# Kernel optimization log

Hardware: AMD Instinct MI355X
Metric: run time of the kernel (lower is better)

## Reference

```python
import jax, jax.numpy as jnp
import numpy as np

# Mamba defaults (mamba_ssm): expand=2, d_state=16, d_conv=4, dt_rank=ceil(d_model/16)
D_MODEL = 256
DEPTH = 2
D_INNER = 2 * D_MODEL          # 512
D_STATE = 16
D_CONV = 4
DT_RANK = (D_MODEL + 15) // 16  # 16
BATCH = 2
SEQLEN = 2048


def setup_inputs() -> dict:
    key = jax.random.key(0)
    ks = jax.random.split(key, 12)
    s = 0.02
    x = jax.random.normal(ks[0], (BATCH, SEQLEN, D_MODEL), jnp.float32)
    ln_w = jnp.ones((DEPTH, D_MODEL), jnp.float32)
    ln_b = jnp.zeros((DEPTH, D_MODEL), jnp.float32)
    in_proj_w = jax.random.normal(ks[1], (DEPTH, 2 * D_INNER, D_MODEL), jnp.float32) * s
    conv_w = jax.random.normal(ks[2], (DEPTH, D_INNER, 1, D_CONV), jnp.float32) * 0.2
    conv_b = jnp.zeros((DEPTH, D_INNER), jnp.float32)
    x_proj_w = jax.random.normal(ks[3], (DEPTH, DT_RANK + 2 * D_STATE, D_INNER), jnp.float32) * s
    dt_proj_w = jax.random.normal(ks[4], (DEPTH, D_INNER, DT_RANK), jnp.float32) * (DT_RANK ** -0.5)
    # dt bias initialized so softplus(bias) ~ U(1e-3, 1e-1), as in mamba_ssm
    dt = jnp.exp(jax.random.uniform(ks[5], (DEPTH, D_INNER)) * (np.log(0.1) - np.log(1e-3)) + np.log(1e-3))
    dt_proj_b = dt + jnp.log(-jnp.expm1(-dt))  # inverse softplus
    A_log = jnp.log(jnp.broadcast_to(jnp.arange(1, D_STATE + 1, dtype=jnp.float32), (DEPTH, D_INNER, D_STATE)))
    D_param = jnp.ones((DEPTH, D_INNER), jnp.float32)
    out_proj_w = jax.random.normal(ks[6], (DEPTH, D_MODEL, D_INNER), jnp.float32) * s
    return {"x": x, "ln_w": ln_w, "ln_b": ln_b, "in_proj_w": in_proj_w,
            "conv_w": conv_w, "conv_b": conv_b, "x_proj_w": x_proj_w,
            "dt_proj_w": dt_proj_w, "dt_proj_b": dt_proj_b, "A_log": A_log,
            "D_param": D_param, "out_proj_w": out_proj_w}


def _layernorm(x, w, b, eps=1e-5):
    mu = jnp.mean(x, axis=-1, keepdims=True)
    var = jnp.var(x, axis=-1, keepdims=True)
    return (x - mu) * jax.lax.rsqrt(var + eps) * w + b


def _mamba_block(x, lw, lb, ipw, cw, cb, xpw, dpw, dpb, alog, dpar, opw):
    # x: [B, L, D]; returns x + Mamba(LN(x))  (residual handled by caller of stack)
    B, L, _ = x.shape
    h = _layernorm(x, lw, lb)
    xz = jnp.einsum('bld,ed->ble', h, ipw)            # [B, L, 2*d_inner]
    xi, z = jnp.split(xz, 2, axis=-1)
    # depthwise causal conv1d
    xc = jnp.transpose(xi, (0, 2, 1))                 # [B, d_inner, L]
    xc = jax.lax.conv_general_dilated(
        xc, cw, window_strides=(1,), padding=[(D_CONV - 1, 0)],
        feature_group_count=D_INNER, dimension_numbers=('NCH', 'OIH', 'NCH'))
    xc = jax.nn.silu(xc + cb[None, :, None])
    xc = jnp.transpose(xc, (0, 2, 1))                 # [B, L, d_inner]
    # input-dependent SSM parameters
    dbl = jnp.einsum('bld,ed->ble', xc, xpw)          # [B, L, dt_rank+2*d_state]
    dt = dbl[..., :DT_RANK]
    Bs = dbl[..., DT_RANK:DT_RANK + D_STATE]          # [B, L, d_state]
    Cs = dbl[..., DT_RANK + D_STATE:]                 # [B, L, d_state]
    delta = jax.nn.softplus(jnp.einsum('blr,dr->bld', dt, dpw) + dpb)  # [B, L, d_inner]
    A = -jnp.exp(alog)                                # [d_inner, d_state]
    dA = jnp.exp(jnp.einsum('bld,dn->bldn', delta, A))
    dBu = jnp.einsum('bld,bln,bld->bldn', delta, Bs, xc)
    # sequential selective scan over time (time-major)
    dA_t = jnp.moveaxis(dA, 1, 0)
    dBu_t = jnp.moveaxis(dBu, 1, 0)
    C_t = jnp.moveaxis(Cs, 1, 0)
    h0 = jnp.zeros((B, D_INNER, D_STATE), x.dtype)
    def step(hprev, inp):
        dA_, dBu_, C_ = inp
        hnew = dA_ * hprev + dBu_                     # [B, d_inner, d_state]
        y = jnp.einsum('bdn,bn->bd', hnew, C_)        # [B, d_inner]
        return hnew, y
    _, ys = jax.lax.scan(step, h0, (dA_t, dBu_t, C_t))
    y = jnp.moveaxis(ys, 0, 1)                        # [B, L, d_inner]
    y = y + xc * dpar
    y = y * jax.nn.silu(z)
    out = jnp.einsum('ble,de->bld', y, opw)           # [B, L, D]
    return x + out


def reference(x, ln_w, ln_b, in_proj_w, conv_w, conv_b, x_proj_w,
              dt_proj_w, dt_proj_b, A_log, D_param, out_proj_w):
    for i in range(DEPTH):
        x = _mamba_block(x, ln_w[i], ln_b[i], in_proj_w[i], conv_w[i], conv_b[i],
                         x_proj_w[i], dt_proj_w[i], dt_proj_b[i], A_log[i],
                         D_param[i], out_proj_w[i])
    return x
```

## Files before the change

### kernel.cpp

```cpp
#include <hip/hip_runtime.h>
#include <hip/hip_bf16.h>
#include <math.h>

#define D_MODEL 256
#define DEPTH 2
#define D_INNER 512
#define D_STATE 16
#define D_CONV 4
#define DT_RANK 16
#define BATCH 2
#define SEQLEN 2048
#define MROWS (BATCH * SEQLEN)

#define LCH 8
#define NCH 512
#define CPB 256

typedef __attribute__((ext_vector_type(8))) short bf16x8;
typedef __attribute__((ext_vector_type(4))) float f32x4;

__device__ __forceinline__ float silu(float v) {
    return v / (1.0f + __expf(-v));
}

__device__ __forceinline__ ushort f2bf(float f) {
    union { float f; unsigned u; } v; v.f = f;
    unsigned r = v.u + 0x7FFFu + ((v.u >> 16) & 1u);
    return (ushort)(r >> 16);
}

__device__ __forceinline__ float bf2f(ushort u) {
    union { unsigned u; float f; } v; v.u = ((unsigned)u) << 16;
    return v.f;
}

__device__ __forceinline__ float softplus_f(float x) {
    return (x > 20.f) ? x : __logf(1.f + __expf(x));
}

#define XS_STR 260
#define HS_STR 264
#define XC_STR 520

__global__ __launch_bounds__(256) void k_cvt(
    const float* __restrict__ ipw, const float* __restrict__ xpw,
    const float* __restrict__ opw, ushort* __restrict__ ipwT,
    ushort* __restrict__ xpwT, ushort* __restrict__ opwT)
{
    size_t tid = (size_t)blockIdx.x * 256 + threadIdx.x;
    {
        int lyr = (int)(tid >> 16), rem = (int)(tid & 65535);
        int n = rem >> 6, k = (rem & 63) * 4;
        float4 v = *(const float4*)(ipw + ((size_t)lyr * 1024 + n) * 256 + k);
        int nt = n >> 4, r = n & 15, kt = k >> 5, c = k & 31;
        ushort4 o = { f2bf(v.x), f2bf(v.y), f2bf(v.z), f2bf(v.w) };
        *(ushort4*)(ipwT + (size_t)lyr * 262144 + (nt * 8 + kt) * 512 + r * 32 + c) = o;
    }
    if (tid < 12288) {
        int lyr = (int)(tid / 6144), rem = (int)(tid % 6144);
        int n = rem >> 7, k = (rem & 127) * 4;
        float4 v = *(const float4*)(xpw + ((size_t)lyr * 48 + n) * 512 + k);
        int nt = n >> 4, r = n & 15, kt = k >> 5, c = k & 31;
        ushort4 o = { f2bf(v.x), f2bf(v.y), f2bf(v.z), f2bf(v.w) };
        *(ushort4*)(xpwT + (size_t)lyr * 24576 + (nt * 16 + kt) * 512 + r * 32 + c) = o;
    }
    if (tid < 65536) {
        int lyr = (int)(tid >> 15), rem = (int)(tid & 32767);
        int n = rem >> 7, k = (rem & 127) * 4;
        float4 v = *(const float4*)(opw + ((size_t)lyr * 256 + n) * 512 + k);
        int nt = n >> 4, r = n & 15, kt = k >> 5, c = k & 31;
        ushort4 o = { f2bf(v.x), f2bf(v.y), f2bf(v.z), f2bf(v.w) };
        *(ushort4*)(opwT + (size_t)lyr * 131072 + (nt * 16 + kt) * 512 + r * 32 + c) = o;
    }
}

__global__ __launch_bounds__(512, 4) void k_front(
    const float* __restrict__ xin, const float* __restrict__ lnwL,
    const float* __restrict__ lnbL, const ushort* __restrict__ ipwT,
    const float* __restrict__ cwL, const float* __restrict__ cbL,
    const ushort* __restrict__ xpwT, const float* __restrict__ dpwL,
    const float* __restrict__ dpbL, const float* __restrict__ alogL,
    ushort* __restrict__ zsB, ushort* __restrict__ xcB,
    float* __restrict__ dbl, float* __restrict__ Ssum,
    float* __restrict__ sdsum)
{
    const int t = threadIdx.x, bid = blockIdx.x;
    const int lane = t & 63, w = t >> 6, l15 = lane & 15, quad = lane >> 4;
    __shared__ float  xs[11 * XS_STR];
    __shared__ ushort hs[16 * HS_STR];
    __shared__ ushort xi_s[11 * 512];
    __shared__ ushort xc_s[16 * XC_STR];
    __shared__ float  dbl_s[8 * 52];
    int m0 = bid * LCH;

    for (int i = t; i < 11 * 64; i += 512) {
        int r = i >> 6, c = (i & 63) * 4;
        int grow = m0 - 3 + r; if (grow < 0) grow = 0;
        float4 v = *(const float4*)(xin + (size_t)grow * D_MODEL + c);
        *(float4*)&xs[r * XS_STR + c] = v;
    }
    __syncthreads();

    if (t < 11 * 32) {
        int r = t >> 5, ci = t & 31;
        float s = 0.f, sq = 0.f;
        #pragma unroll
        for (int k = 0; k < 8; k++) {
            float v = xs[r * XS_STR + ci + 32 * k];
            s += v; sq += v * v;
        }
        #pragma unroll
        for (int off = 1; off < 32; off <<= 1) {
            s  += __shfl_xor(s, off, 32);
            sq += __shfl_xor(sq, off, 32);
        }
        float mu  = s * (1.0f / 256.f);
        float var = sq * (1.0f / 256.f) - mu * mu;
        float rst = rsqrtf(var + 1e-5f);
        #pragma unroll
        for (int k = 0; k < 8; k++) {
            int c = ci + 32 * k;
            float v = (xs[r * XS_STR + c] - mu) * rst * lnwL[c] + lnbL[c];
            hs[r * HS_STR + c] = f2bf(v);
        }
    }
    __syncthreads();

    {
        bf16x8 af[8];
        #pragma unroll
        for (int k8 = 0; k8 < 8; k8++)
            af[k8] = *(const bf16x8*)&hs[l15 * HS_STR + quad * 8 + k8 * 32];
        const ushort* wb = ipwT + (size_t)w * 64 * 512 + l15 * 32 + quad * 8;

        #pragma unroll
        for (int half = 0; half < 2; half++) {
            const ushort* wh = wb + (size_t)half * 4 * 8 * 512;
            f32x4 acc[4];
            #pragma unroll
            for (int f = 0; f < 4; f++) acc[f] = (f32x4){0.f, 0.f, 0.f, 0.f};
            bf16x8 bA[4], bB[4];
            #pragma unroll
            for (int f = 0; f < 4; f++) bA[f] = *(const bf16x8*)(wh + (f * 8) * 512);
            #pragma unroll
            for (int k8 = 0; k8 < 8; k8++) {
                bf16x8* cur = (k8 & 1) ? bB : bA;
                bf16x8* nxt = (k8 & 1) ? bA : bB;
                if (k8 < 7) {
                    #pragma unroll
                    for (int f = 0; f < 4; f++)
                        nxt[f] = *(const bf16x8*)(wh + (f * 8 + k8 + 1) * 512);
                }
                #pragma unroll
                for (int f = 0; f < 4; f++)
                    acc[f] = __builtin_amdgcn_mfma_f32_16x16x32_bf16(af[k8], cur[f], acc[f], 0, 0, 0);
            }
            #pragma unroll
            for (int f = 0; f < 4; f++) {
                int n = w * 128 + (half * 4 + f) * 16 + l15;
                if (n < 512) {
                    #pragma unroll
                    for (int r2 = 0; r2 < 4; r2++) {
                        int rl = quad * 4 + r2;
                        if (rl < 11) xi_s[rl * 512 + n] = f2bf(acc[f][r2]);
                    }
                } else {
                    #pragma unroll
                    for (int r2 = 0; r2 < 4; r2++) {
                        int rl = quad * 4 + r2;
                        if (rl >= 3 && rl < 11)
                            zsB[(size_t)(m0 + rl - 3) * D_INNER + (n - 512)] =
                                f2bf(silu(acc[f][r2]));
                    }
                }
            }
        }
    }
    __syncthreads();

    {
        float4 cw4 = *(const float4*)(cwL + t * 4);
        float cbv = cbL[t];
        #pragma unroll
        for (int rl = 0; rl < LCH; rl++) {
            int l = (m0 + rl) & (SEQLEN - 1);
            float s = cbv;
            if (l >= 3) s = fmaf(cw4.x, bf2f(xi_s[(rl + 0) * 512 + t]), s);
            if (l >= 2) s = fmaf(cw4.y, bf2f(xi_s[(rl + 1) * 512 + t]), s);
            if (l >= 1) s = fmaf(cw4.z, bf2f(xi_s[(rl + 2) * 512 + t]), s);
            s = fmaf(cw4.w, bf2f(xi_s[(rl + 3) * 512 + t]), s);
            ushort xcv = f2bf(silu(s));
            xc_s[rl * XC_STR + t] = xcv;
            xcB[(size_t)(m0 + rl) * D_INNER + t] = xcv;
        }
    }
    __syncthreads();

    if (w < 3) {
        const ushort* wb = xpwT + (size_t)w * 16 * 512 + l15 * 32 + quad * 8;
        bf16x8 bw[16];
        #pragma unroll
        for (int k8 = 0; k8 < 16; k8++)
            bw[k8] = *(const bf16x8*)(wb + k8 * 512);
        f32x4 acc = (f32x4){0.f, 0.f, 0.f, 0.f};
        #pragma unroll
        for (int k8 = 0; k8 < 16; k8++) {
            bf16x8 af = *(const bf16x8*)&xc_s[l15 * XC_STR + quad * 8 + k8 * 32];
            acc = __builtin_amdgcn_mfma_f32_16x16x32_bf16(af, bw[k8], acc, 0, 0, 0);
        }
        int n = w * 16 + l15;
        #pragma unroll
        for (int r2 = 0; r2 < 4; r2++) {
            int rl = quad * 4 + r2;
            if (rl < LCH) {
                dbl_s[rl * 52 + n] = acc[r2];
                dbl[(size_t)(m0 + rl) * 48 + n] = acc[r2];
            }
        }
    }
    __syncthreads();

    {
        float a[16], wdp[16];
        #pragma unroll
        for (int n = 0; n < 16; n++) a[n] = -__expf(alogL[(size_t)t * 16 + n]);
        *(float4*)&wdp[0]  = *(const float4*)(dpwL + (size_t)t * 16 + 0);
        *(float4*)&wdp[4]  = *(const float4*)(dpwL + (size_t)t * 16 + 4);
        *(float4*)&wdp[8]  = *(const float4*)(dpwL + (size_t)t * 16 + 8);
        *(float4*)&wdp[12] = *(const float4*)(dpwL + (size_t)t * 16 + 12);
        float bias = dpbL[t];
        float h[16];
        #pragma unroll
        for (int n = 0; n < 16; n++) h[n] = 0.f;
        float sd = 0.f;
        for (int j = 0; j < LCH; j++) {
            const float* dp = &dbl_s[j * 52];
            float d0 = 0.f, d1 = 0.f;
            #pragma unroll
            for (int r2 = 0; r2 < 8; r2++) {
                d0 = fmaf(dp[r2], wdp[r2], d0);
                d1 = fmaf(dp[8 + r2], wdp[8 + r2], d1);
            }
            float dl = softplus_f(bias + d0 + d1);
            float xv = bf2f(xc_s[j * XC_STR + t]);
            float u = dl * xv;
            sd += dl;
            #pragma unroll
            for (int n = 0; n < 16; n++)
                h[n] = fmaf(__expf(dl * a[n]), h[n], dp[16 + n] * u);
        }
        size_t sbase = (size_t)bid * 16 * D_INNER + t;
        #pragma unroll
        for (int n = 0; n < 16; n++) Ssum[sbase + (size_t)n * D_INNER] = h[n];
        sdsum[(size_t)bid * D_INNER + t] = sd;
    }
}

__global__ __launch_bounds__(512, 4) void k_comb(
    const float* __restrict__ alogL, const float* __restrict__ sdsum,
    float* __restrict__ Ssum)
{
    const int t = threadIdx.x, bid = blockIdx.x;
    __shared__ float S_l[32][17], sd_l[32][17];
    int ch32 = t & 31, seg = t >> 5;
    int chain = bid * 32 + ch32;
    int d = chain & 511;
    int n = (chain >> 9) & 15;
    int b = chain >> 13;
    float a = -__expf(alogL[(size_t)d * 16 + n]);
    int c0 = b * CPB + seg * 16;

    float s_r[16], sd_r[16];
    float S = 0.f, sdt = 0.f;
    #pragma unroll
    for (int j = 0; j < 16; j++) {
        size_t c = (size_t)(c0 + j);
        float s  = Ssum[(c * 16 + n) * D_INNER + d];
        float sd = sdsum[c * D_INNER + d];
        s_r[j] = s; sd_r[j] = sd;
        S = fmaf(__expf(a * sd), S, s);
        sdt += sd;
    }
    S_l[ch32][seg] = S;
    sd_l[ch32][seg] = sdt;
    __syncthreads();

    if (t < 32) {
        float hi = 0.f;
        #pragma unroll
        for (int g = 0; g < 16; g++) {
            float Sv = S_l[t][g], sdv = sd_l[t][g];
            S_l[t][g] = hi;
            hi = fmaf(__expf(a * sdv), hi, Sv);
        }
    }
    __syncthreads();

    float hi = S_l[ch32][seg];
    #pragma unroll
    for (int j = 0; j < 16; j++) {
        size_t c = (size_t)(c0 + j);
        if (!(j & 1))
            Ssum[(c * 16 + n) * D_INNER + d] = hi;
        hi = fmaf(__expf(a * sd_r[j]), hi, s_r[j]);
    }
}

__global__ __launch_bounds__(512, 2) void k_back(
    const float* __restrict__ dbl, const ushort* __restrict__ xcB,
    const ushort* __restrict__ zsB, const float* __restrict__ Ssum,
    const float* __restrict__ dpwL, const float* __restrict__ dpbL,
    const float* __restrict__ alogL, const float* __restrict__ dparL,
    const ushort* __restrict__ opwT, const float* __restrict__ xin,
    float* __restrict__ xout)
{
    const int t = threadIdx.x, bid = blockIdx.x;
    const int lane = t & 63, w = t >> 6, l15 = lane & 15, quad = lane >> 4;
    __shared__ ushort yy_s[16 * XC_STR];
    __shared__ float  dbl_l[16 * 48];
    int m0 = bid * 16;

    for (int i = t; i < 16 * 48; i += 512) dbl_l[i] = dbl[(size_t)m0 * 48 + i];

    ushort xcv[16], zsv[16];
    #pragma unroll
    for (int j = 0; j < 16; j++) {
        size_t rb = (size_t)(m0 + j) * D_INNER + t;
        xcv[j] = xcB[rb];
        zsv[j] = zsB[rb];
    }
    float h[16];
    {
        size_t sbase = ((size_t)(2 * bid) * 16) * D_INNER + t;
        #pragma unroll
        for (int n = 0; n < 16; n++) h[n] = Ssum[sbase + (size_t)n * D_INNER];
    }
    float a[16], wdp[16];
    #pragma unroll
    for (int n = 0; n < 16; n++) a[n] = -__expf(alogL[(size_t)t * 16 + n]);
    *(float4*)&wdp[0]  = *(const float4*)(dpwL + (size_t)t * 16 + 0);
    *(float4*)&wdp[4]  = *(const float4*)(dpwL + (size_t)t * 16 + 4);
    *(float4*)&wdp[8]  = *(const float4*)(dpwL + (size_t)t * 16 + 8);
    *(float4*)&wdp[12] = *(const float4*)(dpwL + (size_t)t * 16 + 12);
    float bias = dpbL[t];
    float Dd = dparL[t];
    __syncthreads();

    for (int j = 0; j < 16; j++) {
        const float* dp = &dbl_l[j * 48];
        float d0 = 0.f, d1 = 0.f;
        #pragma unroll
        for (int r2 = 0; r2 < 8; r2++) {
            d0 = fmaf(dp[r2], wdp[r2], d0);
            d1 = fmaf(dp[8 + r2], wdp[8 + r2], d1);
        }
        float dl = softplus_f(bias + d0 + d1);
        float xv = bf2f(xcv[j]);
        float gate = bf2f(zsv[j]);
        float u = dl * xv;
        float y0 = 0.f, y1 = 0.f, y2 = 0.f, y3 = 0.f;
        #pragma unroll
        for (int q = 0; q < 4; q++) {
            h[4 * q + 0] = fmaf(__expf(dl * a[4 * q + 0]), h[4 * q + 0], dp[16 + 4 * q + 0] * u);
            h[4 * q + 1] = fmaf(__expf(dl * a[4 * q + 1]), h[4 * q + 1], dp[16 + 4 * q + 1] * u);
            h[4 * q + 2] = fmaf(__expf(dl * a[4 * q + 2]), h[4 * q + 2], dp[16 + 4 * q + 2] * u);
            h[4 * q + 3] = fmaf(__expf(dl * a[4 * q + 3]), h[4 * q + 3], dp[16 + 4 * q + 3] * u);
            y0 = fmaf(h[4 * q + 0], dp[32 + 4 * q + 0], y0);
            y1 = fmaf(h[4 * q + 1], dp[32 + 4 * q + 1], y1);
            y2 = fmaf(h[4 * q + 2], dp[32 + 4 * q + 2], y2);
            y3 = fmaf(h[4 * q + 3], dp[32 + 4 * q + 3], y3);
        }
        float y = (y0 + y1) + (y2 + y3) + xv * Dd;
        yy_s[j * XC_STR + t] = f2bf(y * gate);
    }
    __syncthreads();

    {
        const ushort* wb = opwT + (size_t)w * 2 * 16 * 512 + l15 * 32 + quad * 8;
        f32x4 acc0 = (f32x4){0.f, 0.f, 0.f, 0.f};
        f32x4 acc1 = (f32x4){0.f, 0.f, 0.f, 0.f};
        bf16x8 bA0 = *(const bf16x8*)(wb + 0 * 512);
        bf16x8 bA1 = *(const bf16x8*)(wb + 16 * 512);
        bf16x8 bB0, bB1;
        #pragma unroll
        for (int k8 = 0; k8 < 16; k8++) {
            if (k8 < 15) {
                if (k8 & 1) { bA0 = *(const bf16x8*)(wb + (k8 + 1) * 512);
                              bA1 = *(const bf16x8*)(wb + (16 + k8 + 1) * 512); }
                else        { bB0 = *(const bf16x8*)(wb + (k8 + 1) * 512);
                              bB1 = *(const bf16x8*)(wb + (16 + k8 + 1) * 512); }
            }
            bf16x8 af = *(const bf16x8*)&yy_s[l15 * XC_STR + quad * 8 + k8 * 32];
            bf16x8 c0 = (k8 & 1) ? bB0 : bA0;
            bf16x8 c1 = (k8 & 1) ? bB1 : bA1;
            acc0 = __builtin_amdgcn_mfma_f32_16x16x32_bf16(af, c0, acc0, 0, 0, 0);
            acc1 = __builtin_amdgcn_mfma_f32_16x16x32_bf16(af, c1, acc1, 0, 0, 0);
        }
        #pragma unroll
        for (int f = 0; f < 2; f++) {
            int n = w * 32 + f * 16 + l15;
            const f32x4& acc = (f == 0) ? acc0 : acc1;
            #pragma unroll
            for (int r2 = 0; r2 < 4; r2++) {
                int row = m0 + quad * 4 + r2;
                xout[(size_t)row * D_MODEL + n] =
                    acc[r2] + xin[(size_t)row * D_MODEL + n];
            }
        }
    }
}

extern "C" void kernel_launch(void* const* d_in, const int* in_sizes, int n_in,
                              void* d_out, int out_size, void* d_ws, size_t ws_size,
                              hipStream_t stream)
{
    const float* x    = (const float*)d_in[0];
    const float* lnw  = (const float*)d_in[1];
    const float* lnb  = (const float*)d_in[2];
    const float* ipw  = (const float*)d_in[3];
    const float* cw   = (const float*)d_in[4];
    const float* cb   = (const float*)d_in[5];
    const float* xpw  = (const float*)d_in[6];
    const float* dpw  = (const float*)d_in[7];
    const float* dpb  = (const float*)d_in[8];
    const float* alog = (const float*)d_in[9];
    const float* dpar = (const float*)d_in[10];
    const float* opw  = (const float*)d_in[11];
    float* out = (float*)d_out;

    char* p = (char*)d_ws;
    auto alloc = [&](size_t bytes) { char* r = p; p += (bytes + 255) & ~(size_t)255; return r; };
    ushort* zsB   = (ushort*)alloc((size_t)MROWS * D_INNER * 2);
    ushort* xcB   = (ushort*)alloc((size_t)MROWS * D_INNER * 2);
    float*  dbl   = (float*)alloc((size_t)MROWS * 48 * 4);
    float*  Ssum  = (float*)alloc((size_t)NCH * 16 * D_INNER * 4);
    float*  sdsum = (float*)alloc((size_t)NCH * D_INNER * 4);
    ushort* ipwT  = (ushort*)alloc((size_t)DEPTH * 262144 * 2);
    ushort* xpwT  = (ushort*)alloc((size_t)DEPTH * 24576 * 2);
    ushort* opwT  = (ushort*)alloc((size_t)DEPTH * 131072 * 2);

    k_cvt<<<512, 256, 0, stream>>>(ipw, xpw, opw, ipwT, xpwT, opwT);

    for (int lyr = 0; lyr < DEPTH; lyr++) {
        const float* xin = (lyr == 0) ? x : out;
        float* xout = out;
        const float* alogL = alog + (size_t)lyr * D_INNER * D_STATE;
        const float* dpwL  = dpw + (size_t)lyr * D_INNER * DT_RANK;
        const float* dpbL  = dpb + lyr * D_INNER;

        k_front<<<NCH, 512, 0, stream>>>(
            xin, lnw + lyr * D_MODEL, lnb + lyr * D_MODEL,
            ipwT + (size_t)lyr * 262144,
            cw + (size_t)lyr * D_INNER * D_CONV, cb + lyr * D_INNER,
            xpwT + (size_t)lyr * 24576, dpwL, dpbL, alogL,
            zsB, xcB, dbl, Ssum, sdsum);

        k_comb<<<512, 512, 0, stream>>>(alogL, sdsum, Ssum);

        k_back<<<NCH / 2, 512, 0, stream>>>(
            dbl, xcB, zsB, Ssum, dpwL, dpbL, alogL,
            dpar + lyr * D_INNER,
            opwT + (size_t)lyr * 131072, xin, xout);
    }
}
```

Measured before the change: 204.0 us.

## Fuse depthwise causal conv into in_proj MFMA epilogue via lane shuffles

```diff
diff --git a/kernel.cpp b/kernel.cpp
--- a/kernel.cpp
+++ b/kernel.cpp
@@ -88,11 +88,14 @@
     const int lane = t & 63, w = t >> 6, l15 = lane & 15, quad = lane >> 4;
     __shared__ float  xs[11 * XS_STR];
     __shared__ ushort hs[16 * HS_STR];
-    __shared__ ushort xi_s[11 * 512];
     __shared__ ushort xc_s[16 * XC_STR];
     __shared__ float  dbl_s[8 * 52];
+    __shared__ float4 cw_s[512];
+    __shared__ float  cb_s[512];
     int m0 = bid * LCH;
 
+    cw_s[t] = *(const float4*)(cwL + t * 4);
+    cb_s[t] = cbL[t];
     for (int i = t; i < 11 * 64; i += 512) {
         int r = i >> 6, c = (i & 63) * 4;
         int grow = m0 - 3 + r; if (grow < 0) grow = 0;
@@ -155,16 +158,42 @@
                 for (int f = 0; f < 4; f++)
                     acc[f] = __builtin_amdgcn_mfma_f32_16x16x32_bf16(af[k8], cur[f], acc[f], 0, 0, 0);
             }
-            #pragma unroll
-            for (int f = 0; f < 4; f++) {
-                int n = w * 128 + (half * 4 + f) * 16 + l15;
-                if (n < 512) {
-                    #pragma unroll
-                    for (int r2 = 0; r2 < 4; r2++) {
-                        int rl = quad * 4 + r2;
-                        if (rl < 11) xi_s[rl * 512 + n] = f2bf(acc[f][r2]);
+
+            if (w < 4) {
+                #pragma unroll
+                for (int f = 0; f < 4; f++) {
+                    int n = w * 128 + (half * 4 + f) * 16 + l15;
+                    float x0 = acc[f][0], x1 = acc[f][1], x2 = acc[f][2], x3 = acc[f][3];
+                    float p1 = __shfl_up(x1, 16);
+                    float p2 = __shfl_up(x2, 16);
+                    float p3 = __shfl_up(x3, 16);
+                    float4 cwv = cw_s[n];
+                    float cbv = cb_s[n];
+                    int jb = quad * 4 - 3;
+                    #define EMIT(JOFF, T0, T1, T2, T3)                          \
+                    {   int j = jb + (JOFF);                                    \
+                        if (j >= 0 && j < 8) {                                  \
+                            int l = (m0 + j) & (SEQLEN - 1);                    \
+                            float s = cbv;                                      \
+                            if (l >= 3) s = fmaf(cwv.x, (T0), s);               \
+                            if (l >= 2) s = fmaf(cwv.y, (T1), s);               \
+                            if (l >= 1) s = fmaf(cwv.z, (T2), s);               \
+                            s = fmaf(cwv.w, (T3), s);                           \
+                            ushort xv = f2bf(silu(s));                          \
+                            xc_s[j * XC_STR + n] = xv;                          \
+                            xcB[(size_t)(m0 + j) * D_INNER + n] = xv;           \
+                        }                                                       \
                     }
-                } else {
+                    EMIT(0, p1, p2, p3, x0)
+                    EMIT(1, p2, p3, x0, x1)
+                    EMIT(2, p3, x0, x1, x2)
+                    EMIT(3, x0, x1, x2, x3)
+                    #undef EMIT
+                }
+            } else {
+                #pragma unroll
+                for (int f = 0; f < 4; f++) {
+                    int n = w * 128 + (half * 4 + f) * 16 + l15;
                     #pragma unroll
                     for (int r2 = 0; r2 < 4; r2++) {
                         int rl = quad * 4 + r2;
@@ -176,24 +205,22 @@
             }
         }
     }
-    __syncthreads();
-
-    {
-        float4 cw4 = *(const float4*)(cwL + t * 4);
-        float cbv = cbL[t];
-        #pragma unroll
-        for (int rl = 0; rl < LCH; rl++) {
-            int l = (m0 + rl) & (SEQLEN - 1);
-            float s = cbv;
-            if (l >= 3) s = fmaf(cw4.x, bf2f(xi_s[(rl + 0) * 512 + t]), s);
-            if (l >= 2) s = fmaf(cw4.y, bf2f(xi_s[(rl + 1) * 512 + t]), s);
-            if (l >= 1) s = fmaf(cw4.z, bf2f(xi_s[(rl + 2) * 512 + t]), s);
-            s = fmaf(cw4.w, bf2f(xi_s[(rl + 3) * 512 + t]), s);
-            ushort xcv = f2bf(silu(s));
-            xc_s[rl * XC_STR + t] = xcv;
-            xcB[(size_t)(m0 + rl) * D_INNER + t] = xcv;
-        }
-    }
+
+    float a[16], wdp[16];
+    {
+        float al[16];
+        *(float4*)&al[0]   = *(const float4*)(alogL + (size_t)t * 16 + 0);
+        *(float4*)&al[4]   = *(const float4*)(alogL + (size_t)t * 16 + 4);
+        *(float4*)&al[8]   = *(const float4*)(alogL + (size_t)t * 16 + 8);
+        *(float4*)&al[12]  = *(const float4*)(alogL + (size_t)t * 16 + 12);
+        #pragma unroll
+        for (int n = 0; n < 16; n++) a[n] = -__expf(al[n]);
+    }
+    *(float4*)&wdp[0]  = *(const float4*)(dpwL + (size_t)t * 16 + 0);
+    *(float4*)&wdp[4]  = *(const float4*)(dpwL + (size_t)t * 16 + 4);
+    *(float4*)&wdp[8]  = *(const float4*)(dpwL + (size_t)t * 16 + 8);
+    *(float4*)&wdp[12] = *(const float4*)(dpwL + (size_t)t * 16 + 12);
+    float bias = dpbL[t];
     __syncthreads();
 
     if (w < 3) {
@@ -221,14 +248,6 @@
     __syncthreads();
 
     {
-        float a[16], wdp[16];
-        #pragma unroll
-        for (int n = 0; n < 16; n++) a[n] = -__expf(alogL[(size_t)t * 16 + n]);
-        *(float4*)&wdp[0]  = *(const float4*)(dpwL + (size_t)t * 16 + 0);
-        *(float4*)&wdp[4]  = *(const float4*)(dpwL + (size_t)t * 16 + 4);
-        *(float4*)&wdp[8]  = *(const float4*)(dpwL + (size_t)t * 16 + 8);
-        *(float4*)&wdp[12] = *(const float4*)(dpwL + (size_t)t * 16 + 12);
-        float bias = dpbL[t];
         float h[16];
         #pragma unroll
         for (int n = 0; n < 16; n++) h[n] = 0.f;
@@ -336,8 +355,15 @@
         for (int n = 0; n < 16; n++) h[n] = Ssum[sbase + (size_t)n * D_INNER];
     }
     float a[16], wdp[16];
-    #pragma unroll
-    for (int n = 0; n < 16; n++) a[n] = -__expf(alogL[(size_t)t * 16 + n]);
+    {
+        float al[16];
+        *(float4*)&al[0]  = *(const float4*)(alogL + (size_t)t * 16 + 0);
+        *(float4*)&al[4]  = *(const float4*)(alogL + (size_t)t * 16 + 4);
+        *(float4*)&al[8]  = *(const float4*)(alogL + (size_t)t * 16 + 8);
+        *(float4*)&al[12] = *(const float4*)(alogL + (size_t)t * 16 + 12);
+        #pragma unroll
+        for (int n = 0; n < 16; n++) a[n] = -__expf(al[n]);
+    }
     *(float4*)&wdp[0]  = *(const float4*)(dpwL + (size_t)t * 16 + 0);
     *(float4*)&wdp[4]  = *(const float4*)(dpwL + (size_t)t * 16 + 4);
     *(float4*)&wdp[8]  = *(const float4*)(dpwL + (size_t)t * 16 + 8);
```

Measured after the change: 200.0 us. -2.0%, faster.
